# Kernel tuning notes

Hardware: AMD Instinct MI355X
Metric: run time of the kernel (lower is better)

## Reference

```python
import jax, jax.numpy as jnp
import numpy as np

N = 20000   # nodes
E = 320000  # edges per adjacency (avg degree 16)
D = 256     # feature dim


def setup_inputs() -> dict:
    key = jax.random.key(0)
    ks = jax.random.split(key, 7)
    x = jax.random.normal(ks[0], (N, D), dtype=jnp.float32)
    row1 = jax.random.randint(ks[1], (E,), 0, N, dtype=jnp.int32)
    col1 = jax.random.randint(ks[2], (E,), 0, N, dtype=jnp.int32)
    val1 = jax.random.uniform(ks[3], (E,), dtype=jnp.float32)
    row2 = jax.random.randint(ks[4], (E,), 0, N, dtype=jnp.int32)
    col2 = jax.random.randint(ks[5], (E,), 0, N, dtype=jnp.int32)
    val2 = jax.random.uniform(ks[6], (E,), dtype=jnp.float32)
    return {"x": x, "row1": row1, "col1": col1, "val1": val1,
            "row2": row2, "col2": col2, "val2": val2}


def _spmm(row, col, val, x, num_segments):
    # out[i] = sum_{e: row[e]==i} val[e] * x[col[e]]  (COO SpMM)
    msgs = val[:, None] * x[col]           # [E, D] gathered+weighted messages
    return jax.ops.segment_sum(msgs, row, num_segments=num_segments)


def reference(x, row1, col1, val1, row2, col2, val2):
    n = x.shape[0]
    x1 = _spmm(row1, col1, val1, x, n)     # matmul(adj_t, x)
    x2 = _spmm(row2, col2, val2, x, n)     # matmul(adj_t2, x)
    return jnp.concatenate([x1, x2], axis=1)  # [N, 2D]
```

## Files before the change

kernel.cpp:

```cpp
#include <hip/hip_runtime.h>


#define NODES 20000
#define D_FEAT 256
#define OUT_STRIDE (2 * D_FEAT)
#define NR (2 * NODES)
#define REP 8
#define CAP 64
#define SPILL_CAP 16384

typedef float vfloat4 __attribute__((ext_vector_type(4)));
typedef int   vint2   __attribute__((ext_vector_type(2)));
typedef unsigned short vushort8 __attribute__((ext_vector_type(8)));

__device__ __forceinline__ unsigned short f2bf(float f) {
    unsigned u = __float_as_uint(f);
    unsigned r = u + 0x7FFFu + ((u >> 16) & 1u);
    return (unsigned short)(r >> 16);
}
__device__ __forceinline__ float bf2f(unsigned short h) {
    return __uint_as_float((unsigned)h << 16);
}


__global__ __launch_bounds__(256) void k1a_count(
    const int* __restrict__ row1, int E1,
    const int* __restrict__ row2, int E2,
    int* __restrict__ cnt,
    unsigned short* __restrict__ rankl,
    const float* __restrict__ x, unsigned short* __restrict__ xh,
    int edge_blocks, int conv_elems)
{
    if ((int)blockIdx.x < edge_blocks) {
        const int i = blockIdx.x * 256 + threadIdx.x;
        const int Et = E1 + E2;
        if (i >= Et) return;
        const int rj = (i < E1) ? row1[i] : (NODES + row2[i - E1]);
        const int rep = blockIdx.x & (REP - 1);
        rankl[i] = (unsigned short)atomicAdd(&cnt[(size_t)rep * NR + rj], 1);
    } else {
        const int b = blockIdx.x - edge_blocks;
        const long base = ((long)b * 256 + threadIdx.x) * 8;
        if (base >= conv_elems) return;
        const float4 a = reinterpret_cast<const float4*>(x + base)[0];
        const float4 c = reinterpret_cast<const float4*>(x + base)[1];
        vushort8 h;
        h.s0 = f2bf(a.x); h.s1 = f2bf(a.y); h.s2 = f2bf(a.z); h.s3 = f2bf(a.w);
        h.s4 = f2bf(c.x); h.s5 = f2bf(c.y); h.s6 = f2bf(c.z); h.s7 = f2bf(c.w);
        *reinterpret_cast<vushort8*>(xh + base) = h;
    }
}


__global__ __launch_bounds__(256) void k1b_bases(
    int* __restrict__ cnt, int* __restrict__ deg)
{
    const int row = blockIdx.x * 256 + threadIdx.x;
    if (row >= NR) return;
    int run = 0;
    #pragma unroll
    for (int r = 0; r < REP; ++r) {
        const int c = cnt[(size_t)r * NR + row];
        cnt[(size_t)r * NR + row] = run;
        run += c;
    }
    deg[row] = min(run, CAP);
}


__global__ __launch_bounds__(256) void k1c_place(
    const int* __restrict__ row1, const int* __restrict__ col1,
    const float* __restrict__ val1, int E1,
    const int* __restrict__ row2, const int* __restrict__ col2,
    const float* __restrict__ val2, int E2,
    const int* __restrict__ cnt,
    const unsigned short* __restrict__ rankl,
    int2* __restrict__ pairs,
    int* __restrict__ spill_cnt, int4* __restrict__ spill)
{
    const int i = blockIdx.x * 256 + threadIdx.x;
    const int Et = E1 + E2;
    if (i >= Et) return;
    int rj, c; float v;
    if (i < E1) { rj = row1[i];                 c = col1[i]; v = val1[i]; }
    else { const int e = i - E1; rj = NODES + row2[e]; c = col2[e]; v = val2[e]; }
    const int rep = blockIdx.x & (REP - 1);
    const int pos = cnt[(size_t)rep * NR + rj] + (int)rankl[i];
    if (pos < CAP) {
        pairs[(size_t)rj * CAP + pos] = make_int2(c, __float_as_int(v));
    } else {
        const int s = atomicAdd(spill_cnt, 1);
        if (s < SPILL_CAP)
            spill[s] = make_int4(rj, c, __float_as_int(v), 0);
    }
}


__global__ __launch_bounds__(256) void k4_spmm(
    const unsigned short* __restrict__ xh, float* __restrict__ out,
    const int* __restrict__ deg, const int2* __restrict__ pairs,
    const int* __restrict__ spill_cnt, const int4* __restrict__ spill)
{
    const int wid  = threadIdx.x >> 6;
    const int lane = threadIdx.x & 63;
    const int sub  = lane & 31;
    const int hi   = lane >> 5;
    const int r = blockIdx.x * 4 + wid;
    if (r >= NODES) return;
    const int half = blockIdx.y;
    const int rj = half * NODES + r;

    const int dg = deg[rj];
    int c = 0; float v = 0.f;
    if (lane < dg) {
        const vint2 p = __builtin_nontemporal_load(
            reinterpret_cast<const vint2*>(pairs) + (size_t)rj * CAP + lane);
        c = p.x; v = __int_as_float(p.y);
    }

    float a0 = 0.f, a1 = 0.f, a2 = 0.f, a3 = 0.f;
    float a4 = 0.f, a5 = 0.f, a6 = 0.f, a7 = 0.f;

    for (int k = 0; k < dg; k += 8) {
        #pragma unroll
        for (int j = 0; j < 4; ++j) {
            const int e = k + 2 * j + hi;
            const int   ce = __shfl(c, e);
            const float ve = __shfl(v, e);
            const vushort8 h = *reinterpret_cast<const vushort8*>(
                xh + (size_t)ce * D_FEAT + sub * 8);
            a0 += ve * bf2f(h.s0); a1 += ve * bf2f(h.s1);
            a2 += ve * bf2f(h.s2); a3 += ve * bf2f(h.s3);
            a4 += ve * bf2f(h.s4); a5 += ve * bf2f(h.s5);
            a6 += ve * bf2f(h.s6); a7 += ve * bf2f(h.s7);
        }
    }

    const int sc = min(*spill_cnt, SPILL_CAP);
    for (int s = 0; s < sc; ++s) {
        const int4 sp = spill[s];
        if (sp.x == rj) {
            const float sv = hi ? 0.f : __int_as_float(sp.z);
            const vushort8 h = *reinterpret_cast<const vushort8*>(
                xh + (size_t)sp.y * D_FEAT + sub * 8);
            a0 += sv * bf2f(h.s0); a1 += sv * bf2f(h.s1);
            a2 += sv * bf2f(h.s2); a3 += sv * bf2f(h.s3);
            a4 += sv * bf2f(h.s4); a5 += sv * bf2f(h.s5);
            a6 += sv * bf2f(h.s6); a7 += sv * bf2f(h.s7);
        }
    }

    a0 += __shfl_xor(a0, 32); a1 += __shfl_xor(a1, 32);
    a2 += __shfl_xor(a2, 32); a3 += __shfl_xor(a3, 32);
    a4 += __shfl_xor(a4, 32); a5 += __shfl_xor(a5, 32);
    a6 += __shfl_xor(a6, 32); a7 += __shfl_xor(a7, 32);

    vfloat4 st;
    st.x = hi ? a4 : a0;
    st.y = hi ? a5 : a1;
    st.z = hi ? a6 : a2;
    st.w = hi ? a7 : a3;
    vfloat4* dst = reinterpret_cast<vfloat4*>(
        out + (size_t)r * OUT_STRIDE + half * D_FEAT + sub * 8 + hi * 4);
    __builtin_nontemporal_store(st, dst);
}


__global__ __launch_bounds__(256) void spmm_edge_atomic(
    const int* __restrict__ row, const int* __restrict__ col,
    const float* __restrict__ val, const float* __restrict__ x,
    float* __restrict__ out, int num_edges, int col_off)
{
    const int wave_in_block = threadIdx.x >> 6;
    const int lane = threadIdx.x & 63;
    const int e = blockIdx.x * 4 + wave_in_block;
    if (e >= num_edges) return;
    const int r = row[e];
    const int c = col[e];
    const float v = val[e];
    const float4 xv = reinterpret_cast<const float4*>(x + (size_t)c * D_FEAT)[lane];
    float* orow = out + (size_t)r * OUT_STRIDE + col_off + lane * 4;
    atomicAdd(orow + 0, v * xv.x);
    atomicAdd(orow + 1, v * xv.y);
    atomicAdd(orow + 2, v * xv.z);
    atomicAdd(orow + 3, v * xv.w);
}

extern "C" void kernel_launch(void* const* d_in, const int* in_sizes, int n_in,
                              void* d_out, int out_size, void* d_ws, size_t ws_size,
                              hipStream_t stream)
{
    const float* x    = (const float*)d_in[0];
    const int*   row1 = (const int*)d_in[1];
    const int*   col1 = (const int*)d_in[2];
    const float* val1 = (const float*)d_in[3];
    const int*   row2 = (const int*)d_in[4];
    const int*   col2 = (const int*)d_in[5];
    const float* val2 = (const float*)d_in[6];
    float* out = (float*)d_out;

    const int E1 = in_sizes[1];
    const int E2 = in_sizes[4];
    const int Et = E1 + E2;
    const int conv_elems = NODES * D_FEAT;

    const size_t o_cnt   = 0;
    const size_t o_scnt  = o_cnt + (size_t)REP * NR;
    const size_t o_deg   = o_scnt + 4;
    const size_t o_rank  = o_deg + NR;
    const size_t o_spill = (o_rank + ((size_t)Et + 1) / 2 + 3) & ~(size_t)3;
    const size_t o_pairs = o_spill + 4 * (size_t)SPILL_CAP;
    const size_t o_xh    = (o_pairs + 2 * (size_t)NR * CAP + 3) & ~(size_t)3;
    const size_t need_ints = o_xh + (size_t)conv_elems / 2;

    if (ws_size < need_ints * sizeof(int) || (o_pairs & 1) || (o_xh & 3)) {
        (void)hipMemsetAsync(d_out, 0, (size_t)out_size * sizeof(float), stream);
        spmm_edge_atomic<<<dim3((E1 + 3) / 4), 256, 0, stream>>>(
            row1, col1, val1, x, out, E1, 0);
        spmm_edge_atomic<<<dim3((E2 + 3) / 4), 256, 0, stream>>>(
            row2, col2, val2, x, out, E2, D_FEAT);
        return;
    }

    int* w = (int*)d_ws;
    int*  cnt       = w + o_cnt;
    int*  spill_cnt = w + o_scnt;
    int*  deg       = w + o_deg;
    unsigned short* rankl = (unsigned short*)(w + o_rank);
    int4* spill     = (int4*)(w + o_spill);
    int2* pairs     = (int2*)(w + o_pairs);
    unsigned short* xh = (unsigned short*)(w + o_xh);

    (void)hipMemsetAsync(cnt, 0, (o_deg - o_cnt) * sizeof(int), stream);

    const int edge_blocks = (Et + 255) / 256;
    const int conv_blocks = (conv_elems + 256 * 8 - 1) / (256 * 8);
    k1a_count<<<dim3(edge_blocks + conv_blocks), 256, 0, stream>>>(
        row1, E1, row2, E2, cnt, rankl, x, xh, edge_blocks, conv_elems);
    k1b_bases<<<dim3((NR + 255) / 256), 256, 0, stream>>>(cnt, deg);
    k1c_place<<<dim3(edge_blocks), 256, 0, stream>>>(
        row1, col1, val1, E1, row2, col2, val2, E2,
        cnt, rankl, pairs, spill_cnt, spill);
    k4_spmm<<<dim3((NODES + 3) / 4, 2), 256, 0, stream>>>(
        xh, out, deg, pairs, spill_cnt, spill);
}
```

Baseline: 166.4 us.

## Slice bf16 features into 64-wide column panels and split SpMM by slice

The bf16 copy of x is now stored as four column slices of 64 features each, laid out slice-major, so each slice is a contiguous 2.5 MB panel that fits better in cache. The SpMM kernel launches one block per (row group, slice), and each wave processes 8 edges in parallel with 8 lanes per edge covering the 64 features. Partial sums are then reduced with xor shuffles. This aims to improve L2 locality of the random gathers. The cost is that every block reloads the edge pairs and scans the spill list four times, and it adds a three-step shuffle reduction.

```diff
diff --git a/kernel.cpp b/kernel.cpp
--- a/kernel.cpp
+++ b/kernel.cpp
@@ -7,6 +7,8 @@
 #define NR (2 * NODES)
 #define REP 8
 #define CAP 64
+#define NSLICE 4
+#define SLICE_F 64
 #define SPILL_CAP 16384
 
 typedef float vfloat4 __attribute__((ext_vector_type(4)));
@@ -47,7 +49,12 @@
         vushort8 h;
         h.s0 = f2bf(a.x); h.s1 = f2bf(a.y); h.s2 = f2bf(a.z); h.s3 = f2bf(a.w);
         h.s4 = f2bf(c.x); h.s5 = f2bf(c.y); h.s6 = f2bf(c.z); h.s7 = f2bf(c.w);
-        *reinterpret_cast<vushort8*>(xh + base) = h;
+        const long row = base >> 8;
+        const int  d0  = (int)(base & 255);
+        const int  sl  = d0 >> 6;
+        const int  within = d0 & 63;
+        unsigned short* dst = xh + ((size_t)sl * NODES + row) * SLICE_F + within;
+        *reinterpret_cast<vushort8*>(dst) = h;
     }
 }
 
@@ -103,46 +110,46 @@
 {
     const int wid  = threadIdx.x >> 6;
     const int lane = threadIdx.x & 63;
-    const int sub  = lane & 31;
-    const int hi   = lane >> 5;
-    const int r = blockIdx.x * 4 + wid;
-    if (r >= NODES) return;
-    const int half = blockIdx.y;
-    const int rj = half * NODES + r;
-
+    const int slice  = blockIdx.x & (NSLICE - 1);
+    const int rowgrp = blockIdx.x >> 2;
+    const int rj = rowgrp * 4 + wid;
+    if (rj >= NR) return;
+    const int half = (rj >= NODES) ? 1 : 0;
+    const int r = rj - half * NODES;
+
+    const int es = lane >> 3;
+    const int fo = lane & 7;
     const int dg = deg[rj];
-    int c = 0; float v = 0.f;
-    if (lane < dg) {
-        const vint2 p = __builtin_nontemporal_load(
-            reinterpret_cast<const vint2*>(pairs) + (size_t)rj * CAP + lane);
-        c = p.x; v = __int_as_float(p.y);
-    }
+
+    const unsigned short* xbase =
+        xh + (size_t)slice * NODES * SLICE_F + fo * 8;
 
     float a0 = 0.f, a1 = 0.f, a2 = 0.f, a3 = 0.f;
     float a4 = 0.f, a5 = 0.f, a6 = 0.f, a7 = 0.f;
 
     for (int k = 0; k < dg; k += 8) {
-        #pragma unroll
-        for (int j = 0; j < 4; ++j) {
-            const int e = k + 2 * j + hi;
-            const int   ce = __shfl(c, e);
-            const float ve = __shfl(v, e);
-            const vushort8 h = *reinterpret_cast<const vushort8*>(
-                xh + (size_t)ce * D_FEAT + sub * 8);
-            a0 += ve * bf2f(h.s0); a1 += ve * bf2f(h.s1);
-            a2 += ve * bf2f(h.s2); a3 += ve * bf2f(h.s3);
-            a4 += ve * bf2f(h.s4); a5 += ve * bf2f(h.s5);
-            a6 += ve * bf2f(h.s6); a7 += ve * bf2f(h.s7);
+        const int slot = k + es;
+        int c = 0; float v = 0.f;
+        if (slot < dg) {
+            const vint2 p = __builtin_nontemporal_load(
+                reinterpret_cast<const vint2*>(pairs) + (size_t)rj * CAP + slot);
+            c = p.x; v = __int_as_float(p.y);
         }
+        const vushort8 h = *reinterpret_cast<const vushort8*>(
+            xbase + (size_t)c * SLICE_F);
+        a0 += v * bf2f(h.s0); a1 += v * bf2f(h.s1);
+        a2 += v * bf2f(h.s2); a3 += v * bf2f(h.s3);
+        a4 += v * bf2f(h.s4); a5 += v * bf2f(h.s5);
+        a6 += v * bf2f(h.s6); a7 += v * bf2f(h.s7);
     }
 
     const int sc = min(*spill_cnt, SPILL_CAP);
     for (int s = 0; s < sc; ++s) {
         const int4 sp = spill[s];
-        if (sp.x == rj) {
-            const float sv = hi ? 0.f : __int_as_float(sp.z);
+        if (sp.x == rj && es == 0) {
+            const float sv = __int_as_float(sp.z);
             const vushort8 h = *reinterpret_cast<const vushort8*>(
-                xh + (size_t)sp.y * D_FEAT + sub * 8);
+                xbase + (size_t)sp.y * SLICE_F);
             a0 += sv * bf2f(h.s0); a1 += sv * bf2f(h.s1);
             a2 += sv * bf2f(h.s2); a3 += sv * bf2f(h.s3);
             a4 += sv * bf2f(h.s4); a5 += sv * bf2f(h.s5);
@@ -150,19 +157,23 @@
         }
     }
 
-    a0 += __shfl_xor(a0, 32); a1 += __shfl_xor(a1, 32);
-    a2 += __shfl_xor(a2, 32); a3 += __shfl_xor(a3, 32);
-    a4 += __shfl_xor(a4, 32); a5 += __shfl_xor(a5, 32);
-    a6 += __shfl_xor(a6, 32); a7 += __shfl_xor(a7, 32);
-
-    vfloat4 st;
-    st.x = hi ? a4 : a0;
-    st.y = hi ? a5 : a1;
-    st.z = hi ? a6 : a2;
-    st.w = hi ? a7 : a3;
-    vfloat4* dst = reinterpret_cast<vfloat4*>(
-        out + (size_t)r * OUT_STRIDE + half * D_FEAT + sub * 8 + hi * 4);
-    __builtin_nontemporal_store(st, dst);
+    #pragma unroll
+    for (int d = 8; d < 64; d <<= 1) {
+        a0 += __shfl_xor(a0, d); a1 += __shfl_xor(a1, d);
+        a2 += __shfl_xor(a2, d); a3 += __shfl_xor(a3, d);
+        a4 += __shfl_xor(a4, d); a5 += __shfl_xor(a5, d);
+        a6 += __shfl_xor(a6, d); a7 += __shfl_xor(a7, d);
+    }
+
+    if (es == 0) {
+        float* orow = out + (size_t)r * OUT_STRIDE + half * D_FEAT
+                      + slice * SLICE_F + fo * 8;
+        vfloat4 lo, hi2;
+        lo.x = a0; lo.y = a1; lo.z = a2; lo.w = a3;
+        hi2.x = a4; hi2.y = a5; hi2.z = a6; hi2.w = a7;
+        __builtin_nontemporal_store(lo,  reinterpret_cast<vfloat4*>(orow));
+        __builtin_nontemporal_store(hi2, reinterpret_cast<vfloat4*>(orow + 4));
+    }
 }
 
 
@@ -241,6 +252,6 @@
     k1c_place<<<dim3(edge_blocks), 256, 0, stream>>>(
         row1, col1, val1, E1, row2, col2, val2, E2,
         cnt, rankl, pairs, spill_cnt, spill);
-    k4_spmm<<<dim3((NODES + 3) / 4, 2), 256, 0, stream>>>(
+    k4_spmm<<<dim3(NR), 256, 0, stream>>>(
         xh, out, deg, pairs, spill_cnt, spill);
 }
```

After: 204.2 us. 22.7% more time.
